# Performance work log

Measured on AMD Instinct MI355X. Metric: run time of the kernel, lower is better.

Reference implementation:

```python
import jax, jax.numpy as jnp
import numpy as np

SYM_LIST = (0,)  # from init_kwargs sym_list=[0]
N_PTS = 16384


def setup_inputs() -> dict:
    key = jax.random.key(0)
    k1, k2, k3, k4 = jax.random.split(key, 4)
    pred_R = jax.random.normal(k1, (1, 3, 3), dtype=jnp.float32)
    pred_t = jax.random.normal(k2, (1, 3), dtype=jnp.float32)
    pts_model = jax.random.normal(k3, (1, N_PTS, 3), dtype=jnp.float32)
    pts_gt = jax.random.normal(k4, (1, N_PTS, 3), dtype=jnp.float32)
    return {
        "pred_R": pred_R,
        "pred_t": pred_t,
        "pts_model": pts_model,
        "pts_gt": pts_gt,
        "model_index": 0,
    }


def reference(pred_R, pred_t, pts_model, pts_gt, model_index):
    # pose transform: pts_pred[b,n,:] = R[b] @ pts_model[b,n,:] + t[b]
    pts_pred = jnp.einsum("bij,bnj->bni", pred_R, pts_model) + pred_t[:, None, :]

    if int(model_index) in SYM_LIST:
        # bs == 1 in the symmetric branch (matches pts_gt[0] in the original)
        p = pts_pred[0]  # (N, 3) predicted points (queries)
        g = pts_gt[0]    # (N, 3) ground-truth points (references)
        # brute-force 1-NN: squared pairwise distances (N, N)
        d2 = (
            jnp.sum(p * p, axis=-1)[:, None]
            - 2.0 * (p @ g.T)
            + jnp.sum(g * g, axis=-1)[None, :]
        )
        idx = jnp.argmin(d2, axis=1)          # nearest gt point per predicted point
        g_nn = jnp.take(g, idx, axis=0)       # gather (N, 3)
        pts_gt_matched = g_nn[None, :, :]
        pts_pred = p[None, :, :]
    else:
        pts_gt_matched = pts_gt

    # mean L2 distance per batch element -> shape (bs,)
    diff = pts_pred - pts_gt_matched
    dis_loss = jnp.mean(jnp.sqrt(jnp.sum(diff * diff, axis=2)), axis=1)
    return dis_loss
```

## Files before the change

kernel.cpp:

```cpp
#include <hip/hip_runtime.h>
#include <math.h>

#define N_PTS 16384
#define WAVE_P 128
#define BLK_P  512
#define NPB    (N_PTS / BLK_P)
#define CHUNK_G 512
#define NCH    (N_PTS / CHUNK_G)
#define NGROUP (CHUNK_G / 32)
#define NFBLK  64

typedef __attribute__((ext_vector_type(8)))  short short8_t;
typedef __attribute__((ext_vector_type(16))) float f32x16;

__device__ __forceinline__ unsigned short bf_rn(float x) {
    unsigned u = __float_as_uint(x);
    unsigned r = (u + 0x7fffu + ((u >> 16) & 1u)) >> 16;
    return (unsigned short)r;
}
__device__ __forceinline__ float bf_up(unsigned short s) {
    return __uint_as_float(((unsigned)s) << 16);
}
__device__ __forceinline__ unsigned enc_f32(float f) {
    unsigned b = __float_as_uint(f);
    return (b & 0x80000000u) ? ~b : (b | 0x80000000u);
}
__device__ __forceinline__ float dec_f32(unsigned k) {
    unsigned b = (k & 0x80000000u) ? (k & 0x7fffffffu) : ~k;
    return __uint_as_float(b);
}
__device__ __forceinline__ float min3f(float a, float b, float c) {
    return fminf(fminf(a, b), c);
}

__global__ __launch_bounds__(256) void k_prep(
        const float* __restrict__ R, const float* __restrict__ t,
        const float* __restrict__ m, const float* __restrict__ g,
        float4* __restrict__ pws, float4* __restrict__ gws,
        float* __restrict__ ppv,
        unsigned short* __restrict__ paA, unsigned short* __restrict__ pbB,
        unsigned* __restrict__ keys) {
    int n = blockIdx.x * 256 + threadIdx.x;
    keys[n] = 0xFFFFFFFFu;

    float mx = m[3*n+0], my = m[3*n+1], mz = m[3*n+2];
    float px = fmaf(R[0], mx, fmaf(R[1], my, R[2]*mz)) + t[0];
    float py = fmaf(R[3], mx, fmaf(R[4], my, R[5]*mz)) + t[1];
    float pz = fmaf(R[6], mx, fmaf(R[7], my, R[8]*mz)) + t[2];
    float pp = fmaf(px,px,fmaf(py,py,pz*pz));
    pws[n] = make_float4(-2.f*px, -2.f*py, -2.f*pz, pp);
    ppv[n] = pp;
    float gx = g[3*n+0], gy = g[3*n+1], gz = g[3*n+2];
    float gg = fmaf(gx,gx,fmaf(gy,gy,gz*gz));
    gws[n] = make_float4(gx, gy, gz, gg);

    float Px = -2.f*px, Py = -2.f*py, Pz = -2.f*pz;
    unsigned short phx = bf_rn(Px), phy = bf_rn(Py), phz = bf_rn(Pz);
    unsigned short plx = bf_rn(Px - bf_up(phx)),
                   ply = bf_rn(Py - bf_up(phy)),
                   plz = bf_rn(Pz - bf_up(phz));
    unsigned short ghx = bf_rn(gx), ghy = bf_rn(gy), ghz = bf_rn(gz);
    unsigned short glx = bf_rn(gx - bf_up(ghx)),
                   gly = bf_rn(gy - bf_up(ghy)),
                   glz = bf_rn(gz - bf_up(ghz));
    unsigned short ggh = bf_rn(gg), ggl = bf_rn(gg - bf_up(ggh));
    const unsigned short one = 0x3F80;

    union { unsigned short u[16]; int4 v[2]; } A, B;
    A.u[0]=ghx; A.u[1]=ghy; A.u[2]=ghz; A.u[3]=ghx; A.u[4]=ghy; A.u[5]=ghz;
    A.u[6]=ggh; A.u[7]=ggl; A.u[8]=glx; A.u[9]=gly; A.u[10]=glz;
    A.u[11]=0; A.u[12]=0; A.u[13]=0; A.u[14]=0; A.u[15]=0;
    B.u[0]=phx; B.u[1]=phy; B.u[2]=phz; B.u[3]=plx; B.u[4]=ply; B.u[5]=plz;
    B.u[6]=one; B.u[7]=one; B.u[8]=phx; B.u[9]=phy; B.u[10]=phz;
    B.u[11]=0; B.u[12]=0; B.u[13]=0; B.u[14]=0; B.u[15]=0;

    int4* pa = (int4*)(paA + (size_t)n * 16);
    int4* pb = (int4*)(pbB + (size_t)n * 16);
    pa[0] = A.v[0]; pa[1] = A.v[1];
    pb[0] = B.v[0]; pb[1] = B.v[1];
}

__device__ __forceinline__ float tree16c(f32x16 d, float carry) {
    float m0 = min3f(d[0],  d[1],  d[2]);
    float m1 = min3f(d[3],  d[4],  d[5]);
    float m2 = min3f(d[6],  d[7],  d[8]);
    float m3 = min3f(d[9],  d[10], d[11]);
    float m4 = min3f(d[12], d[13], d[14]);
    float m5 = min3f(m4, d[15], carry);
    return min3f(m0, m1, min3f(m2, m3, m5));
}

__global__ __launch_bounds__(256) void k_nn_mfma(
        const unsigned short* __restrict__ paA,
        const unsigned short* __restrict__ pbB,
        unsigned* __restrict__ keys) {
    const int tid = threadIdx.x;
    const int wid = tid >> 6, l = tid & 63;
    const int lc = l & 31, lh = l >> 5;
    const int pbase = blockIdx.x * BLK_P + wid * WAVE_P;
    const int g0 = blockIdx.y * CHUNK_G;

    short8_t B0 = *(const short8_t*)(pbB + (size_t)(pbase +  0 + lc)*16 + lh*8);
    short8_t B1 = *(const short8_t*)(pbB + (size_t)(pbase + 32 + lc)*16 + lh*8);
    short8_t B2 = *(const short8_t*)(pbB + (size_t)(pbase + 64 + lc)*16 + lh*8);
    short8_t B3 = *(const short8_t*)(pbB + (size_t)(pbase + 96 + lc)*16 + lh*8);

    const f32x16 zc = {};
    float rm0 = 3.4e38f, rm1 = 3.4e38f, rm2 = 3.4e38f, rm3 = 3.4e38f;

    const unsigned short* aptr = paA + (size_t)(g0 + lc)*16 + lh*8;
    short8_t a = *(const short8_t*)aptr;
    #pragma unroll 2
    for (int gi = 0; gi < NGROUP; ++gi) {
        short8_t an = (gi + 1 < NGROUP)
                      ? *(const short8_t*)(aptr + (size_t)(gi + 1) * 512) : a;
        {
            f32x16 d0 = __builtin_amdgcn_mfma_f32_32x32x16_bf16(a, B0, zc, 0, 0, 0);
            f32x16 d1 = __builtin_amdgcn_mfma_f32_32x32x16_bf16(a, B1, zc, 0, 0, 0);
            rm0 = tree16c(d0, rm0);
            rm1 = tree16c(d1, rm1);
        }
        {
            f32x16 d2 = __builtin_amdgcn_mfma_f32_32x32x16_bf16(a, B2, zc, 0, 0, 0);
            f32x16 d3 = __builtin_amdgcn_mfma_f32_32x32x16_bf16(a, B3, zc, 0, 0, 0);
            rm2 = tree16c(d2, rm2);
            rm3 = tree16c(d3, rm3);
        }
        a = an;
    }

    rm0 = fminf(rm0, __shfl_xor(rm0, 32, 64));
    rm1 = fminf(rm1, __shfl_xor(rm1, 32, 64));
    rm2 = fminf(rm2, __shfl_xor(rm2, 32, 64));
    rm3 = fminf(rm3, __shfl_xor(rm3, 32, 64));

    if (lh == 0) {
        atomicMin(&keys[pbase + lc],      enc_f32(rm0));
        atomicMin(&keys[pbase + 32 + lc], enc_f32(rm1));
        atomicMin(&keys[pbase + 64 + lc], enc_f32(rm2));
        atomicMin(&keys[pbase + 96 + lc], enc_f32(rm3));
    }
}

__global__ __launch_bounds__(256, 4) void k_nn_vec(
        const float4* __restrict__ pws, const float4* __restrict__ gws,
        unsigned* __restrict__ keys) {
    const int tid = threadIdx.x;
    const int pbase = blockIdx.x * 2048;
    const int g0 = blockIdx.y * 64;
    float px[8], py[8], pz[8], sm[8];
    #pragma unroll
    for (int k = 0; k < 8; ++k) {
        float4 p = pws[pbase + k*256 + tid];
        px[k]=p.x; py[k]=p.y; pz[k]=p.z; sm[k]=3.4e38f;
    }
    #pragma unroll 4
    for (int gi = 0; gi < 64; gi += 2) {
        float4 a = gws[g0 + gi];
        float4 b = gws[g0 + gi + 1];
        #pragma unroll
        for (int k = 0; k < 8; ++k) {
            float sa = fmaf(px[k], a.x, fmaf(py[k], a.y, fmaf(pz[k], a.z, a.w)));
            float sb = fmaf(px[k], b.x, fmaf(py[k], b.y, fmaf(pz[k], b.z, b.w)));
            sm[k] = fminf(sm[k], fminf(sa, sb));
        }
    }
    #pragma unroll
    for (int k = 0; k < 8; ++k)
        atomicMin(&keys[pbase + k*256 + tid], enc_f32(sm[k]));
}

__global__ __launch_bounds__(256) void k_fin(
        const float* __restrict__ R, const float* __restrict__ t,
        const float* __restrict__ m, const float* __restrict__ g,
        const float* __restrict__ ppv, const unsigned* __restrict__ keys,
        const int* __restrict__ midx, float* __restrict__ psum) {
    const int tid = threadIdx.x;
    const int n = blockIdx.x * 256 + tid;
    const bool sym = (midx[0] == 0);
    float dis;
    if (sym) {
        float d2 = ppv[n] + dec_f32(keys[n]);
        dis = sqrtf(fmaxf(d2, 0.f));
    } else {
        float mx=m[3*n+0], my=m[3*n+1], mz=m[3*n+2];
        float dx = fmaf(R[0],mx,fmaf(R[1],my,R[2]*mz)) + t[0] - g[3*n+0];
        float dy = fmaf(R[3],mx,fmaf(R[4],my,R[5]*mz)) + t[1] - g[3*n+1];
        float dz = fmaf(R[6],mx,fmaf(R[7],my,R[8]*mz)) + t[2] - g[3*n+2];
        dis = sqrtf(fmaf(dx,dx,fmaf(dy,dy,dz*dz)));
    }
    #pragma unroll
    for (int off = 32; off > 0; off >>= 1) dis += __shfl_down(dis, off, 64);
    __shared__ float sred[4];
    if ((tid & 63) == 0) sred[tid >> 6] = dis;
    __syncthreads();
    if (tid == 0) psum[blockIdx.x] = (sred[0] + sred[1]) + (sred[2] + sred[3]);
}

__global__ void k_final(const float* __restrict__ psum, float* __restrict__ out) {
    float v = psum[threadIdx.x];
    #pragma unroll
    for (int off = 32; off > 0; off >>= 1) v += __shfl_down(v, off, 64);
    if (threadIdx.x == 0) out[0] = v / (float)N_PTS;
}

extern "C" void kernel_launch(void* const* d_in, const int* in_sizes, int n_in,
                              void* d_out, int out_size, void* d_ws, size_t ws_size,
                              hipStream_t stream) {
    const float* R   = (const float*)d_in[0];
    const float* t   = (const float*)d_in[1];
    const float* m   = (const float*)d_in[2];
    const float* g   = (const float*)d_in[3];
    const int* midx  = (const int*)d_in[4];

    char* ws = (char*)d_ws;
    float* out = (float*)d_out;

    unsigned* keys = (unsigned*)ws;
    float*    psum = (float*)(ws + 65536);
    float*    ppv  = (float*)(ws + 65536 + 1024);
    float4*   pws  = (float4*)(ws + 65536 + 1024 + 65536);
    float4*   gws  = (float4*)(ws + 65536 + 1024 + 65536 + 262144);
    unsigned short* paA = (unsigned short*)(ws + 65536 + 1024 + 65536 + 524288);
    unsigned short* pbB = paA + (size_t)16 * N_PTS;
    const size_t need = 65536 + 1024 + 65536 + 524288 + 1048576;

    k_prep<<<dim3(N_PTS/256), dim3(256), 0, stream>>>(
        R, t, m, g, pws, gws, ppv, paA, pbB, keys);

    if (ws_size >= need) {
        k_nn_mfma<<<dim3(NPB, NCH), dim3(256), 0, stream>>>(paA, pbB, keys);
    } else {
        k_nn_vec<<<dim3(8, 256), dim3(256), 0, stream>>>(pws, gws, keys);
    }

    k_fin<<<dim3(NFBLK), dim3(256), 0, stream>>>(
        R, t, m, g, ppv, keys, midx, psum);
    k_final<<<dim3(1), dim3(64), 0, stream>>>(psum, out);
}
```

Measured before the change: 25.92 us.

## Fuse prep into MFMA NN kernel with LDS-staged gt chunk and partial-min buffer

Drops the separate prep kernel. Each NN block now builds its own bf16 hi/lo gt operands in shared memory and computes the transformed query operands in registers. Per-chunk minima go to a partial buffer (NCH x N) instead of using atomicMin, and the final kernel reduces across chunks and recomputes |p|^2. This removes one launch and the global round-trip for packed operands, at the cost of redundant per-block operand preparation and a 32-way reduction in the finish kernel.

Result: slower. 28.71 us (+10.8%).

```diff
diff --git a/kernel.cpp b/kernel.cpp
--- a/kernel.cpp
+++ b/kernel.cpp
@@ -8,6 +8,7 @@
 #define CHUNK_G 512
 #define NCH    (N_PTS / CHUNK_G)
 #define NGROUP (CHUNK_G / 32)
+#define ROWS   24
 #define NFBLK  64
 
 typedef __attribute__((ext_vector_type(8)))  short short8_t;
@@ -32,52 +33,13 @@
 __device__ __forceinline__ float min3f(float a, float b, float c) {
     return fminf(fminf(a, b), c);
 }
-
-__global__ __launch_bounds__(256) void k_prep(
-        const float* __restrict__ R, const float* __restrict__ t,
-        const float* __restrict__ m, const float* __restrict__ g,
-        float4* __restrict__ pws, float4* __restrict__ gws,
-        float* __restrict__ ppv,
-        unsigned short* __restrict__ paA, unsigned short* __restrict__ pbB,
-        unsigned* __restrict__ keys) {
-    int n = blockIdx.x * 256 + threadIdx.x;
-    keys[n] = 0xFFFFFFFFu;
-
-    float mx = m[3*n+0], my = m[3*n+1], mz = m[3*n+2];
-    float px = fmaf(R[0], mx, fmaf(R[1], my, R[2]*mz)) + t[0];
-    float py = fmaf(R[3], mx, fmaf(R[4], my, R[5]*mz)) + t[1];
-    float pz = fmaf(R[6], mx, fmaf(R[7], my, R[8]*mz)) + t[2];
-    float pp = fmaf(px,px,fmaf(py,py,pz*pz));
-    pws[n] = make_float4(-2.f*px, -2.f*py, -2.f*pz, pp);
-    ppv[n] = pp;
-    float gx = g[3*n+0], gy = g[3*n+1], gz = g[3*n+2];
-    float gg = fmaf(gx,gx,fmaf(gy,gy,gz*gz));
-    gws[n] = make_float4(gx, gy, gz, gg);
-
-    float Px = -2.f*px, Py = -2.f*py, Pz = -2.f*pz;
-    unsigned short phx = bf_rn(Px), phy = bf_rn(Py), phz = bf_rn(Pz);
-    unsigned short plx = bf_rn(Px - bf_up(phx)),
-                   ply = bf_rn(Py - bf_up(phy)),
-                   plz = bf_rn(Pz - bf_up(phz));
-    unsigned short ghx = bf_rn(gx), ghy = bf_rn(gy), ghz = bf_rn(gz);
-    unsigned short glx = bf_rn(gx - bf_up(ghx)),
-                   gly = bf_rn(gy - bf_up(ghy)),
-                   glz = bf_rn(gz - bf_up(ghz));
-    unsigned short ggh = bf_rn(gg), ggl = bf_rn(gg - bf_up(ggh));
-    const unsigned short one = 0x3F80;
-
-    union { unsigned short u[16]; int4 v[2]; } A, B;
-    A.u[0]=ghx; A.u[1]=ghy; A.u[2]=ghz; A.u[3]=ghx; A.u[4]=ghy; A.u[5]=ghz;
-    A.u[6]=ggh; A.u[7]=ggl; A.u[8]=glx; A.u[9]=gly; A.u[10]=glz;
-    A.u[11]=0; A.u[12]=0; A.u[13]=0; A.u[14]=0; A.u[15]=0;
-    B.u[0]=phx; B.u[1]=phy; B.u[2]=phz; B.u[3]=plx; B.u[4]=ply; B.u[5]=plz;
-    B.u[6]=one; B.u[7]=one; B.u[8]=phx; B.u[9]=phy; B.u[10]=phz;
-    B.u[11]=0; B.u[12]=0; B.u[13]=0; B.u[14]=0; B.u[15]=0;
-
-    int4* pa = (int4*)(paA + (size_t)n * 16);
-    int4* pb = (int4*)(pbB + (size_t)n * 16);
-    pa[0] = A.v[0]; pa[1] = A.v[1];
-    pb[0] = B.v[0]; pb[1] = B.v[1];
+__device__ __forceinline__ short8_t pack8(unsigned short a0, unsigned short a1,
+        unsigned short a2, unsigned short a3, unsigned short a4,
+        unsigned short a5, unsigned short a6, unsigned short a7) {
+    union { unsigned short u[8]; short8_t v; } x;
+    x.u[0]=a0; x.u[1]=a1; x.u[2]=a2; x.u[3]=a3;
+    x.u[4]=a4; x.u[5]=a5; x.u[6]=a6; x.u[7]=a7;
+    return x.v;
 }
 
 __device__ __forceinline__ float tree16c(f32x16 d, float carry) {
@@ -90,39 +52,78 @@
     return min3f(m0, m1, min3f(m2, m3, m5));
 }
 
-__global__ __launch_bounds__(256) void k_nn_mfma(
-        const unsigned short* __restrict__ paA,
-        const unsigned short* __restrict__ pbB,
-        unsigned* __restrict__ keys) {
+template<bool ATOMIC>
+__global__ __launch_bounds__(256) void k_nn_fused(
+        const float* __restrict__ R, const float* __restrict__ t,
+        const float* __restrict__ m, const float* __restrict__ g,
+        float* __restrict__ partial ) {
+    __shared__ unsigned short sgA[CHUNK_G * ROWS];
     const int tid = threadIdx.x;
     const int wid = tid >> 6, l = tid & 63;
     const int lc = l & 31, lh = l >> 5;
     const int pbase = blockIdx.x * BLK_P + wid * WAVE_P;
-    const int g0 = blockIdx.y * CHUNK_G;
-
-    short8_t B0 = *(const short8_t*)(pbB + (size_t)(pbase +  0 + lc)*16 + lh*8);
-    short8_t B1 = *(const short8_t*)(pbB + (size_t)(pbase + 32 + lc)*16 + lh*8);
-    short8_t B2 = *(const short8_t*)(pbB + (size_t)(pbase + 64 + lc)*16 + lh*8);
-    short8_t B3 = *(const short8_t*)(pbB + (size_t)(pbase + 96 + lc)*16 + lh*8);
+    const int gch = blockIdx.y * CHUNK_G;
+
+    const float r0=R[0], r1=R[1], r2=R[2], r3=R[3], r4=R[4],
+                r5=R[5], r6=R[6], r7=R[7], r8=R[8];
+    const float t0=t[0], t1=t[1], t2=t[2];
+
+    #pragma unroll
+    for (int k = 0; k < 2; ++k) {
+        int r = k * 256 + tid;
+        int n = gch + r;
+        float gx = g[3*n+0], gy = g[3*n+1], gz = g[3*n+2];
+        float gg = fmaf(gx,gx,fmaf(gy,gy,gz*gz));
+        unsigned short ghx = bf_rn(gx), ghy = bf_rn(gy), ghz = bf_rn(gz);
+        unsigned short glx = bf_rn(gx - bf_up(ghx)),
+                       gly = bf_rn(gy - bf_up(ghy)),
+                       glz = bf_rn(gz - bf_up(ghz));
+        unsigned short ggh = bf_rn(gg), ggl = bf_rn(gg - bf_up(ggh));
+        short8_t h0 = pack8(ghx, ghy, ghz, ghx, ghy, ghz, ggh, ggl);
+        short8_t h1 = pack8(glx, gly, glz, 0, 0, 0, 0, 0);
+        *(short8_t*)(sgA + (size_t)r * ROWS)     = h0;
+        *(short8_t*)(sgA + (size_t)r * ROWS + 8) = h1;
+    }
+
+    short8_t Bf[4];
+    #pragma unroll
+    for (int f = 0; f < 4; ++f) {
+        int n = pbase + f * 32 + lc;
+        float mx = m[3*n+0], my = m[3*n+1], mz = m[3*n+2];
+        float px = fmaf(r0,mx,fmaf(r1,my,r2*mz)) + t0;
+        float py = fmaf(r3,mx,fmaf(r4,my,r5*mz)) + t1;
+        float pz = fmaf(r6,mx,fmaf(r7,my,r8*mz)) + t2;
+        float Px = -2.f*px, Py = -2.f*py, Pz = -2.f*pz;
+        unsigned short phx = bf_rn(Px), phy = bf_rn(Py), phz = bf_rn(Pz);
+        if (lh == 0) {
+            unsigned short plx = bf_rn(Px - bf_up(phx)),
+                           ply = bf_rn(Py - bf_up(phy)),
+                           plz = bf_rn(Pz - bf_up(phz));
+            Bf[f] = pack8(phx, phy, phz, plx, ply, plz, 0x3F80, 0x3F80);
+        } else {
+            Bf[f] = pack8(phx, phy, phz, 0, 0, 0, 0, 0);
+        }
+    }
+    __syncthreads();
 
     const f32x16 zc = {};
     float rm0 = 3.4e38f, rm1 = 3.4e38f, rm2 = 3.4e38f, rm3 = 3.4e38f;
 
-    const unsigned short* aptr = paA + (size_t)(g0 + lc)*16 + lh*8;
-    short8_t a = *(const short8_t*)aptr;
+    const unsigned short* abase = sgA + (size_t)lc * ROWS + lh * 8;
+    short8_t a = *(const short8_t*)abase;
     #pragma unroll 2
     for (int gi = 0; gi < NGROUP; ++gi) {
         short8_t an = (gi + 1 < NGROUP)
-                      ? *(const short8_t*)(aptr + (size_t)(gi + 1) * 512) : a;
+                      ? *(const short8_t*)(abase + (size_t)(gi + 1) * 32 * ROWS) : a;
         {
-            f32x16 d0 = __builtin_amdgcn_mfma_f32_32x32x16_bf16(a, B0, zc, 0, 0, 0);
-            f32x16 d1 = __builtin_amdgcn_mfma_f32_32x32x16_bf16(a, B1, zc, 0, 0, 0);
+            f32x16 d0 = __builtin_amdgcn_mfma_f32_32x32x16_bf16(a, Bf[0], zc, 0, 0, 0);
+            f32x16 d1 = __builtin_amdgcn_mfma_f32_32x32x16_bf16(a, Bf[1], zc, 0, 0, 0);
             rm0 = tree16c(d0, rm0);
             rm1 = tree16c(d1, rm1);
         }
         {
-            f32x16 d2 = __builtin_amdgcn_mfma_f32_32x32x16_bf16(a, B2, zc, 0, 0, 0);
-            f32x16 d3 = __builtin_amdgcn_mfma_f32_32x32x16_bf16(a, B3, zc, 0, 0, 0);
+            f32x16 d2 = __builtin_amdgcn_mfma_f32_32x32x16_bf16(a, Bf[2], zc, 0, 0, 0);
+            f32x16 d3 = __builtin_amdgcn_mfma_f32_32x32x16_bf16(a, Bf[3], zc, 0, 0, 0);
             rm2 = tree16c(d2, rm2);
             rm3 = tree16c(d3, rm3);
         }
@@ -135,58 +136,52 @@
     rm3 = fminf(rm3, __shfl_xor(rm3, 32, 64));
 
     if (lh == 0) {
-        atomicMin(&keys[pbase + lc],      enc_f32(rm0));
-        atomicMin(&keys[pbase + 32 + lc], enc_f32(rm1));
-        atomicMin(&keys[pbase + 64 + lc], enc_f32(rm2));
-        atomicMin(&keys[pbase + 96 + lc], enc_f32(rm3));
-    }
-}
-
-__global__ __launch_bounds__(256, 4) void k_nn_vec(
-        const float4* __restrict__ pws, const float4* __restrict__ gws,
-        unsigned* __restrict__ keys) {
-    const int tid = threadIdx.x;
-    const int pbase = blockIdx.x * 2048;
-    const int g0 = blockIdx.y * 64;
-    float px[8], py[8], pz[8], sm[8];
-    #pragma unroll
-    for (int k = 0; k < 8; ++k) {
-        float4 p = pws[pbase + k*256 + tid];
-        px[k]=p.x; py[k]=p.y; pz[k]=p.z; sm[k]=3.4e38f;
-    }
-    #pragma unroll 4
-    for (int gi = 0; gi < 64; gi += 2) {
-        float4 a = gws[g0 + gi];
-        float4 b = gws[g0 + gi + 1];
-        #pragma unroll
-        for (int k = 0; k < 8; ++k) {
-            float sa = fmaf(px[k], a.x, fmaf(py[k], a.y, fmaf(pz[k], a.z, a.w)));
-            float sb = fmaf(px[k], b.x, fmaf(py[k], b.y, fmaf(pz[k], b.z, b.w)));
-            sm[k] = fminf(sm[k], fminf(sa, sb));
-        }
-    }
-    #pragma unroll
-    for (int k = 0; k < 8; ++k)
-        atomicMin(&keys[pbase + k*256 + tid], enc_f32(sm[k]));
-}
-
+        if (ATOMIC) {
+            unsigned* keys = (unsigned*)partial;
+            atomicMin(&keys[pbase + lc],      enc_f32(rm0));
+            atomicMin(&keys[pbase + 32 + lc], enc_f32(rm1));
+            atomicMin(&keys[pbase + 64 + lc], enc_f32(rm2));
+            atomicMin(&keys[pbase + 96 + lc], enc_f32(rm3));
+        } else {
+            float* row = partial + (size_t)blockIdx.y * N_PTS + pbase + lc;
+            row[0]  = rm0;
+            row[32] = rm1;
+            row[64] = rm2;
+            row[96] = rm3;
+        }
+    }
+}
+
+template<bool ATOMIC>
 __global__ __launch_bounds__(256) void k_fin(
         const float* __restrict__ R, const float* __restrict__ t,
         const float* __restrict__ m, const float* __restrict__ g,
-        const float* __restrict__ ppv, const unsigned* __restrict__ keys,
-        const int* __restrict__ midx, float* __restrict__ psum) {
+        const float* __restrict__ partial, const int* __restrict__ midx,
+        float* __restrict__ psum) {
     const int tid = threadIdx.x;
     const int n = blockIdx.x * 256 + tid;
     const bool sym = (midx[0] == 0);
+
+    float mx = m[3*n+0], my = m[3*n+1], mz = m[3*n+2];
+    float px = fmaf(R[0],mx,fmaf(R[1],my,R[2]*mz)) + t[0];
+    float py = fmaf(R[3],mx,fmaf(R[4],my,R[5]*mz)) + t[1];
+    float pz = fmaf(R[6],mx,fmaf(R[7],my,R[8]*mz)) + t[2];
+
     float dis;
     if (sym) {
-        float d2 = ppv[n] + dec_f32(keys[n]);
-        dis = sqrtf(fmaxf(d2, 0.f));
+        float smin;
+        if (ATOMIC) {
+            smin = dec_f32(((const unsigned*)partial)[n]);
+        } else {
+            smin = 3.4e38f;
+            #pragma unroll 8
+            for (int c = 0; c < NCH; ++c)
+                smin = fminf(smin, partial[(size_t)c * N_PTS + n]);
+        }
+        float pp = fmaf(px,px,fmaf(py,py,pz*pz));
+        dis = sqrtf(fmaxf(pp + smin, 0.f));
     } else {
-        float mx=m[3*n+0], my=m[3*n+1], mz=m[3*n+2];
-        float dx = fmaf(R[0],mx,fmaf(R[1],my,R[2]*mz)) + t[0] - g[3*n+0];
-        float dy = fmaf(R[3],mx,fmaf(R[4],my,R[5]*mz)) + t[1] - g[3*n+1];
-        float dz = fmaf(R[6],mx,fmaf(R[7],my,R[8]*mz)) + t[2] - g[3*n+2];
+        float dx = px - g[3*n+0], dy = py - g[3*n+1], dz = pz - g[3*n+2];
         dis = sqrtf(fmaf(dx,dx,fmaf(dy,dy,dz*dz)));
     }
     #pragma unroll
@@ -216,25 +211,23 @@
     char* ws = (char*)d_ws;
     float* out = (float*)d_out;
 
-    unsigned* keys = (unsigned*)ws;
-    float*    psum = (float*)(ws + 65536);
-    float*    ppv  = (float*)(ws + 65536 + 1024);
-    float4*   pws  = (float4*)(ws + 65536 + 1024 + 65536);
-    float4*   gws  = (float4*)(ws + 65536 + 1024 + 65536 + 262144);
-    unsigned short* paA = (unsigned short*)(ws + 65536 + 1024 + 65536 + 524288);
-    unsigned short* pbB = paA + (size_t)16 * N_PTS;
-    const size_t need = 65536 + 1024 + 65536 + 524288 + 1048576;
-
-    k_prep<<<dim3(N_PTS/256), dim3(256), 0, stream>>>(
-        R, t, m, g, pws, gws, ppv, paA, pbB, keys);
-
-    if (ws_size >= need) {
-        k_nn_mfma<<<dim3(NPB, NCH), dim3(256), 0, stream>>>(paA, pbB, keys);
+    const size_t partial_bytes = (size_t)NCH * N_PTS * 4;
+    if (ws_size >= partial_bytes + 1024) {
+        float* partial = (float*)ws;
+        float* psum    = (float*)(ws + partial_bytes);
+        k_nn_fused<false><<<dim3(NPB, NCH), dim3(256), 0, stream>>>(
+            R, t, m, g, partial);
+        k_fin<false><<<dim3(NFBLK), dim3(256), 0, stream>>>(
+            R, t, m, g, partial, midx, psum);
+        k_final<<<dim3(1), dim3(64), 0, stream>>>(psum, out);
     } else {
-        k_nn_vec<<<dim3(8, 256), dim3(256), 0, stream>>>(pws, gws, keys);
-    }
-
-    k_fin<<<dim3(NFBLK), dim3(256), 0, stream>>>(
-        R, t, m, g, ppv, keys, midx, psum);
-    k_final<<<dim3(1), dim3(64), 0, stream>>>(psum, out);
-}
+        unsigned* keys = (unsigned*)ws;
+        float*    psum = (float*)(ws + (size_t)N_PTS * 4);
+        hipMemsetAsync(keys, 0xFF, (size_t)N_PTS * 4, stream);
+        k_nn_fused<true><<<dim3(NPB, NCH), dim3(256), 0, stream>>>(
+            R, t, m, g, (float*)keys);
+        k_fin<true><<<dim3(NFBLK), dim3(256), 0, stream>>>(
+            R, t, m, g, (const float*)keys, midx, psum);
+        k_final<<<dim3(1), dim3(64), 0, stream>>>(psum, out);
+    }
+}
```
